# Kernel tuning notes

Measured on AMD Instinct MI355X. Metric: run time of the kernel, lower is better.

## Reference

```python
import math
import jax, jax.numpy as jnp
import numpy as np

NUM_HEAD = 16


def setup_inputs() -> dict:
    key = jax.random.key(0)
    k1, k2, k3, k4 = jax.random.split(key, 4)
    B, N, E = 64, 577, 1024
    x = jax.random.normal(k1, (B, N, E), dtype=jnp.float32)
    # nn.Linear weights are [out, in]; applied as x @ W.T. Scale like torch init.
    s = 1.0 / math.sqrt(E)
    Wq = jax.random.normal(k2, (E, E), dtype=jnp.float32) * s
    Wk = jax.random.normal(k3, (E, E), dtype=jnp.float32) * s
    Wv = jax.random.normal(k4, (E, E), dtype=jnp.float32) * s
    return {"x": x, "Wq": Wq, "Wk": Wk, "Wv": Wv}


def reference(x, Wq, Wk, Wv):
    B, N, E = x.shape
    H = NUM_HEAD
    D = E // H
    # QKV projections (bias=False), split heads -> [B, H, N, D]
    def proj(W):
        return (x @ W.T).reshape(B, N, H, D).transpose(0, 2, 1, 3)
    q, k, v = proj(Wq), proj(Wk), proj(Wv)
    # scaled dot-product attention (eval mode: dropout_p = 0)
    scale = 1.0 / math.sqrt(D)
    scores = jnp.einsum("bhnd,bhmd->bhnm", q, k) * scale
    probs = jax.nn.softmax(scores, axis=-1)
    out = jnp.einsum("bhnm,bhmd->bhnd", probs, v)
    # merge heads -> [B, N, E]
    return out.transpose(0, 2, 1, 3).reshape(B, N, E)
```

## Files before the change

### kernel.cpp

```cpp
#include <hip/hip_runtime.h>
#include <hip/hip_bf16.h>


typedef __attribute__((ext_vector_type(8))) short s16x8;
typedef __attribute__((ext_vector_type(4))) float f32x4;
typedef __attribute__((ext_vector_type(16))) float f32x16;
typedef __attribute__((ext_vector_type(4))) unsigned int u32x4;
typedef __attribute__((ext_vector_type(2))) unsigned int u32x2;

#define MFMA16(a, b, c) __builtin_amdgcn_mfma_f32_16x16x32_bf16((a), (b), (c), 0, 0, 0)
#define MFMA32(a, b, c) __builtin_amdgcn_mfma_f32_32x32x16_bf16((a), (b), (c), 0, 0, 0)

__device__ __forceinline__ short f2bf(float f) {
    unsigned u = __builtin_bit_cast(unsigned, f);
    u += 0x7FFFu + ((u >> 16) & 1u);
    return (short)(u >> 16);
}

__device__ __forceinline__ unsigned cvtpk(float lo, float hi) {
    unsigned r;
    asm("v_cvt_pk_bf16_f32 %0, %1, %2" : "=v"(r) : "v"(lo), "v"(hi));
    return r;
}

__device__ __forceinline__ void gload_lds16(const void* g, void* l) {
    __builtin_amdgcn_global_load_lds(
        (const __attribute__((address_space(1))) unsigned int*)g,
        (__attribute__((address_space(3))) unsigned int*)l,
        16, 0, 0);
}

__global__ __launch_bounds__(256) void convert_bf16(
    const float* __restrict__ x,
    const float* __restrict__ Wq,
    const float* __restrict__ Wk,
    const float* __restrict__ Wv,
    short* __restrict__ xb,
    short* __restrict__ Wb)
{
    constexpr size_t NX = 37814272u / 8u;
    constexpr size_t NW = 1048576u / 8u;
    constexpr size_t NTOT = NX + 3u * NW;
    size_t stride = (size_t)gridDim.x * blockDim.x;
    for (size_t c = (size_t)blockIdx.x * blockDim.x + threadIdx.x; c < NTOT; c += stride) {
        const float* src;
        short* dst;
        size_t off;
        if (c < NX) { src = x; off = c * 8; dst = xb + off; }
        else {
            size_t cw = c - NX;
            int wsel = (int)(cw / NW);
            src = (wsel == 0) ? Wq : (wsel == 1) ? Wk : Wv;
            off = (cw - (size_t)wsel * NW) * 8;
            dst = Wb + cw * 8;
        }
        float4 a0 = *reinterpret_cast<const float4*>(src + off);
        float4 a1 = *reinterpret_cast<const float4*>(src + off + 4);
        s16x8 v;
        v[0]=f2bf(a0.x); v[1]=f2bf(a0.y); v[2]=f2bf(a0.z); v[3]=f2bf(a0.w);
        v[4]=f2bf(a1.x); v[5]=f2bf(a1.y); v[6]=f2bf(a1.z); v[7]=f2bf(a1.w);
        *reinterpret_cast<s16x8*>(dst) = v;
    }
}

__global__ __launch_bounds__(512, 2) void qkv_gemm4(
    const short* __restrict__ xb,
    const short* __restrict__ Wb,
    short* __restrict__ Qb,
    short* __restrict__ Kb,
    short* __restrict__ Vb)
{
    constexpr int M = 36928;
    constexpr int NT = 12;
    constexpr int NWG = 145 * NT;
    __shared__ char LDS[131072];

    const int t    = threadIdx.x;
    const int lane = t & 63;
    const int w    = t >> 6;
    const int wr   = w >> 2, wc = w & 3;
    const int ml   = lane & 15, zz = lane >> 4;

    int orig = blockIdx.x;
    int xcd  = orig & 7;
    constexpr int QO = NWG / 8, RO = NWG % 8;
    int id = (xcd < RO ? xcd * (QO + 1) : RO * (QO + 1) + (xcd - RO) * QO) + (orig >> 3);
    const int tileM = (id / NT) * 256;
    const int tileN = (id % NT) * 256;

    const char* Ab = (const char*)xb;
    const char* Bb = (const char*)Wb;

    int s_row[2], s_lcol[2], s_arow[2];
    #pragma unroll
    for (int p = 0; p < 2; ++p) {
        int u = p * 512 + t;
        int row = u >> 2;
        int physu = u & 3;
        s_row[p]  = row;
        s_lcol[p] = ((physu ^ ((row >> 1) & 3)) << 4);
        int ar = tileM + row; if (ar > M - 1) ar = M - 1;
        s_arow[p] = ar;
    }

    #define REGOFF(buf_, op_, ks_) ((buf_) * 65536 + (op_) * 32768 + (ks_) * 16384)

    #define STAGE(tt_, op_, ks_, buf_)                                          \
    {   _Pragma("unroll")                                                       \
        for (int p = 0; p < 2; ++p) {                                           \
            int u = p * 512 + t;                                                \
            size_t gb;                                                          \
            if ((op_) == 0) gb = (size_t)s_arow[p] * 2048 + (tt_) * 128 + (ks_) * 64 + s_lcol[p]; \
            else            gb = (size_t)(tileN + s_row[p]) * 2048 + (tt_) * 128 + (ks_) * 64 + s_lcol[p]; \
            gload_lds16((((op_) == 0) ? Ab : Bb) + gb,                          \
                        LDS + REGOFF(buf_, op_, ks_) + u * 16);                 \
        } }

    auto rdA = [&](int buf, int ks, int mf) {
        int row = wr * 128 + mf * 16 + ml;
        int off = REGOFF(buf, 0, ks) + row * 64 + ((zz ^ ((row >> 1) & 3)) << 4);
        return *reinterpret_cast<const s16x8*>(LDS + off);
    };
    auto rdB = [&](int buf, int ks, int nf) {
        int row = wc * 64 + nf * 16 + ml;
        int off = REGOFF(buf, 1, ks) + row * 64 + ((zz ^ ((row >> 1) & 3)) << 4);
        return *reinterpret_cast<const s16x8*>(LDS + off);
    };

    #define RD_A(dst_, buf_, mb_)                                  \
    {   _Pragma("unroll")                                          \
        for (int mf2 = 0; mf2 < 4; ++mf2) {                        \
            dst_[mf2*2+0] = rdA(buf_, 0, (mb_)+mf2);               \
            dst_[mf2*2+1] = rdA(buf_, 1, (mb_)+mf2);               \
        } }
    #define RD_B(dst_, buf_, nb_)                                  \
    {   _Pragma("unroll")                                          \
        for (int nf2 = 0; nf2 < 2; ++nf2) {                        \
            dst_[nf2*2+0] = rdB(buf_, 0, (nb_)+nf2);               \
            dst_[nf2*2+1] = rdB(buf_, 1, (nb_)+nf2);               \
        } }

    #define QMFMA(AF_, BF_, MH_, NH_)                              \
    {   __builtin_amdgcn_s_setprio(1);                             \
        _Pragma("unroll")                                          \
        for (int mf2 = 0; mf2 < 4; ++mf2)                          \
            _Pragma("unroll")                                      \
            for (int nf2 = 0; nf2 < 2; ++nf2)                      \
                acc[(MH_)*4+mf2][(NH_)*2+nf2] =                    \
                    MFMA16(AF_[mf2*2+0], BF_[nf2*2+0], acc[(MH_)*4+mf2][(NH_)*2+nf2]); \
        _Pragma("unroll")                                          \
        for (int mf2 = 0; mf2 < 4; ++mf2)                          \
            _Pragma("unroll")                                      \
            for (int nf2 = 0; nf2 < 2; ++nf2)                      \
                acc[(MH_)*4+mf2][(NH_)*2+nf2] =                    \
                    MFMA16(AF_[mf2*2+1], BF_[nf2*2+1], acc[(MH_)*4+mf2][(NH_)*2+nf2]); \
        __builtin_amdgcn_s_setprio(0); }

    f32x4 acc[8][4] = {};
    s16x8 aC[8], aN[8], bC[4], bN[4];

    STAGE(0, 0, 0, 0); STAGE(0, 1, 0, 0); STAGE(0, 0, 1, 0); STAGE(0, 1, 1, 0);
    asm volatile("s_waitcnt vmcnt(0)" ::: "memory");
    __builtin_amdgcn_s_barrier();
    __builtin_amdgcn_sched_barrier(0);
    RD_A(aC, 0, 0);
    RD_B(bC, 0, 0);

    for (int tt = 0; tt < 16; ++tt) {
        const int buf = tt & 1, nbuf = buf ^ 1;
        const bool pre = (tt < 15);

        asm volatile("s_waitcnt lgkmcnt(0)" ::: "memory");
        __builtin_amdgcn_sched_barrier(0);
        if (pre) { STAGE(tt + 1, 0, 0, nbuf); STAGE(tt + 1, 1, 0, nbuf); }
        RD_B(bN, buf, 2);
        RD_A(aN, buf, 4);
        QMFMA(aC, bC, 0, 0);

        asm volatile("s_waitcnt lgkmcnt(8)" ::: "memory");
        __builtin_amdgcn_sched_barrier(0);
        if (pre) { STAGE(tt + 1, 0, 1, nbuf); STAGE(tt + 1, 1, 1, nbuf); }
        QMFMA(aC, bN, 0, 1);

        asm volatile("s_waitcnt lgkmcnt(0)" ::: "memory");
        __builtin_amdgcn_sched_barrier(0);
        QMFMA(aN, bC, 1, 0);

        asm volatile("s_waitcnt vmcnt(0)" ::: "memory");
        __builtin_amdgcn_s_barrier();
        __builtin_amdgcn_sched_barrier(0);
        if (pre) { RD_A(aC, nbuf, 0); RD_B(bC, nbuf, 0); }
        QMFMA(aN, bN, 1, 1);
    }

    const int z2 = tileN >> 10;
    short* Ob = (z2 == 0) ? Qb : (z2 == 1) ? Kb : Vb;
    const int cbase = (tileN & 1023) + wc * 64;

    #pragma unroll
    for (int mf = 0; mf < 8; ++mf) {
        #pragma unroll
        for (int j = 0; j < 4; ++j) {
            int row = tileM + wr * 128 + mf * 16 + zz * 4 + j;
            if (row < M) {
                int b = row / 577;
                int n = row - b * 577;
                #pragma unroll
                for (int nf = 0; nf < 4; ++nf) {
                    int cz = cbase + nf * 16 + ml;
                    int h = cz >> 6, dd = cz & 63;
                    Ob[(((size_t)(b * 16 + h)) * 577 + n) * 64 + dd] = f2bf(acc[mf][nf][j]);
                }
            }
        }
    }
    #undef STAGE
    #undef REGOFF
    #undef RD_A
    #undef RD_B
    #undef QMFMA
}

__global__ __launch_bounds__(256) void vtrans(
    const short* __restrict__ Vb,
    short* __restrict__ Vt)
{
    __shared__ short lds[64 * 64];
    const int t  = threadIdx.x;
    const int n0 = blockIdx.x * 64;
    const int bh = blockIdx.y;
    const size_t slab  = (size_t)bh * (577 * 64);
    const size_t vslab = (size_t)bh * (64 * 584);

    int r  = t >> 2;
    int d0 = (t & 3) * 16;
    int row = n0 + r; if (row > 576) row = 576;
    const short* src = Vb + slab + (size_t)row * 64 + d0;
    s16x8 v0 = *reinterpret_cast<const s16x8*>(src);
    s16x8 v1 = *reinterpret_cast<const s16x8*>(src + 8);
    #pragma unroll
    for (int j = 0; j < 8; ++j) {
        lds[(d0 + j) * 64 + r]     = v0[j];
        lds[(d0 + 8 + j) * 64 + r] = v1[j];
    }
    __syncthreads();
    #pragma unroll
    for (int p = 0; p < 2; ++p) {
        int u  = p * 256 + t;
        int dd = u >> 3, ns = u & 7;
        int n  = n0 + ns * 8;
        if (n < 584) {
            s16x8 vv = *reinterpret_cast<const s16x8*>(&lds[dd * 64 + ns * 8]);
            *reinterpret_cast<s16x8*>(Vt + vslab + (size_t)dd * 584 + n) = vv;
        }
    }
}

__global__ __launch_bounds__(256, 4) void attn_fwd5(
    const short* __restrict__ Qb,
    const short* __restrict__ Kb,
    const short* __restrict__ Vt,
    float* __restrict__ out)
{
    constexpr int   N    = 577;
    constexpr float CEXP = 0.18033688011112042f;

    __shared__ short K_lds[2][4096];
    __shared__ short V_lds[2][4096];

    const int t     = threadIdx.x;
    const int lane  = t & 63;
    const int w     = t >> 6;
    const int col_q = lane & 31;
    const int hi    = lane >> 5;
    const int hi8   = hi * 8;
    const int c7    = col_q & 7;

    int bd  = blockIdx.x;
    int xx  = bd & 7;
    int r_  = bd >> 3;
    int qt  = r_ % 5;
    int bh  = (r_ / 5) * 8 + xx;
    const int bB = bh >> 4, hH = bh & 15;
    const size_t slab  = (size_t)bh * (N * 64);
    const size_t vslab = (size_t)bh * (64 * 584);

    const int q0 = qt * 128 + w * 32;

    s16x8 qb[4];
    {
        int qr = q0 + col_q; if (qr > N - 1) qr = N - 1;
        const short* qrow = Qb + slab + (size_t)qr * 64 + hi8;
        #pragma unroll
        for (int ks = 0; ks < 4; ++ks)
            qb[ks] = *reinterpret_cast<const s16x8*>(qrow + ks * 16);
    }

    const int sr = t >> 3;
    const int sp = t & 7;

    float m_run = -1e30f, l_run = 0.f;
    f32x16 o0 = {}, o1 = {};

    #pragma unroll
    for (int p = 0; p < 2; ++p) {
        int rr = p * 32 + sr;
        int sl = sp ^ (rr & 7);
        gload_lds16(Kb + slab + (size_t)rr * 64 + sl * 8, &K_lds[0][(rr * 8 + sp) * 8]);
        gload_lds16(Vt + vslab + (size_t)rr * 584 + sl * 8, &V_lds[0][(rr * 8 + sp) * 8]);
    }
    int cur = 0;

    for (int tile = 0; tile < 10; ++tile) {
        const int kv0 = tile * 64;
        __builtin_amdgcn_sched_barrier(0);
        __builtin_amdgcn_s_barrier();
        if (tile < 9) {
            #pragma unroll
            for (int p = 0; p < 2; ++p) {
                int rr = p * 32 + sr;
                int sl = sp ^ (rr & 7);
                gload_lds16(Kb + slab + (size_t)(kv0 + 64 + rr) * 64 + sl * 8,
                            &K_lds[cur ^ 1][(rr * 8 + sp) * 8]);
                gload_lds16(Vt + vslab + (size_t)rr * 584 + (kv0 + 64) + sl * 8,
                            &V_lds[cur ^ 1][(rr * 8 + sp) * 8]);
            }
            asm volatile("s_waitcnt vmcnt(4)" ::: "memory");
        } else {
            asm volatile("s_waitcnt vmcnt(0)" ::: "memory");
        }
        __builtin_amdgcn_sched_barrier(0);

        const short* KL = &K_lds[cur][0];
        const short* VL = &V_lds[cur][0];

        f32x16 s0 = {}, s1 = {};
        __builtin_amdgcn_s_setprio(1);
        #pragma unroll
        for (int ks = 0; ks < 4; ++ks) {
            s16x8 kf0 = *reinterpret_cast<const s16x8*>(
                KL + ((col_q * 8 + ((2*ks + hi) ^ c7)) * 8));
            s0 = MFMA32(kf0, qb[ks], s0);
        }
        #pragma unroll
        for (int ks = 0; ks < 4; ++ks) {
            s16x8 kf1 = *reinterpret_cast<const s16x8*>(
                KL + (((32 + col_q) * 8 + ((2*ks + hi) ^ c7)) * 8));
            s1 = MFMA32(kf1, qb[ks], s1);
        }
        __builtin_amdgcn_s_setprio(0);

        if (kv0 + 64 > N) {
            #pragma unroll
            for (int r = 0; r < 16; ++r) {
                int crow = (r & 3) + 8 * (r >> 2) + 4 * hi;
                if (kv0 + crow > N - 1) s0[r] = -1e30f;
                s1[r] = -1e30f;
            }
        }

        float pm = s0[0];
        #pragma unroll
        for (int r = 1; r < 15; r += 2) pm = fmaxf(fmaxf(pm, s0[r]), s0[r+1]);
        pm = fmaxf(pm, s0[15]);
        #pragma unroll
        for (int r = 0; r < 16; r += 2) pm = fmaxf(fmaxf(pm, s1[r]), s1[r+1]);
        float pmax2 = fmaxf(pm, __shfl_xor(pm, 32));

        bool need = (pmax2 - m_run) * CEXP > 8.f;
        if (__ballot(need)) {
            float mn   = fmaxf(m_run, pmax2);
            float corr = exp2f(CEXP * (m_run - mn));
            m_run = mn;
            l_run *= corr;
            #pragma unroll
            for (int r = 0; r < 16; ++r) { o0[r] *= corr; o1[r] *= corr; }
        }
        float cmn = CEXP * m_run;

        float psum = 0.f;
        #pragma unroll
        for (int r = 0; r < 16; ++r) { s0[r] = exp2f(__builtin_fmaf(s0[r], CEXP, -cmn)); psum += s0[r]; }
        #pragma unroll
        for (int r = 0; r < 16; ++r) { s1[r] = exp2f(__builtin_fmaf(s1[r], CEXP, -cmn)); psum += s1[r]; }
        l_run += psum + __shfl_xor(psum, 32);

        #define REPACK(S_, b_, dst_)                                              \
        {   u32x2 r1_ = __builtin_amdgcn_permlane32_swap(                         \
                cvtpk(S_[(b_)+0], S_[(b_)+1]), cvtpk(S_[(b_)+4], S_[(b_)+5]), false, false); \
            u32x2 r2_ = __builtin_amdgcn_permlane32_swap(                         \
                cvtpk(S_[(b_)+2], S_[(b_)+3]), cvtpk(S_[(b_)+6], S_[(b_)+7]), false, false); \
            dst_[0] = r1_[0]; dst_[2] = r1_[1]; dst_[1] = r2_[0]; dst_[3] = r2_[1]; }

        #define PVSTEP(ks_, S_, b_)                                               \
        {   u32x4 pwk_;                                                           \
            REPACK(S_, b_, pwk_);                                                 \
            s16x8 paf_ = __builtin_bit_cast(s16x8, pwk_);                         \
            s16x8 vf0_ = *reinterpret_cast<const s16x8*>(                         \
                VL + ((col_q * 8 + ((2*(ks_) + hi) ^ c7)) * 8));                  \
            o0 = MFMA32(vf0_, paf_, o0);                                          \
            s16x8 vf1_ = *reinterpret_cast<const s16x8*>(                         \
                VL + (((32 + col_q) * 8 + ((2*(ks_) + hi) ^ c7)) * 8));           \
            o1 = MFMA32(vf1_, paf_, o1);                                          \
        }

        __builtin_amdgcn_s_setprio(1);
        PVSTEP(0, s0, 0)
        PVSTEP(1, s0, 8)
        PVSTEP(2, s1, 0)
        PVSTEP(3, s1, 8)
        __builtin_amdgcn_s_setprio(0);
        #undef PVSTEP
        #undef REPACK
        cur ^= 1;
    }

    int q = q0 + col_q;
    if (q < N) {
        float inv = 1.0f / l_run;
        float* obase = out + ((size_t)bB * 577 + q) * 1024 + (size_t)hH * 64;
        #pragma unroll
        for (int gq = 0; gq < 4; ++gq) {
            float4 v0 = { o0[4*gq+0]*inv, o0[4*gq+1]*inv, o0[4*gq+2]*inv, o0[4*gq+3]*inv };
            *reinterpret_cast<float4*>(obase + 8*gq + 4*hi) = v0;
            float4 v1 = { o1[4*gq+0]*inv, o1[4*gq+1]*inv, o1[4*gq+2]*inv, o1[4*gq+3]*inv };
            *reinterpret_cast<float4*>(obase + 32 + 8*gq + 4*hi) = v1;
        }
    }
}

extern "C" void kernel_launch(void* const* d_in, const int* in_sizes, int n_in,
                              void* d_out, int out_size, void* d_ws, size_t ws_size,
                              hipStream_t stream) {
    const float* x  = (const float*)d_in[0];
    const float* Wq = (const float*)d_in[1];
    const float* Wk = (const float*)d_in[2];
    const float* Wv = (const float*)d_in[3];
    float* out = (float*)d_out;

    const size_t SZ   = (size_t)64 * 16 * 577 * 64 * 2;
    const size_t VTSZ = (size_t)1024 * 64 * 584 * 2;
    short* Qb = (short*)d_ws;
    short* Kb = (short*)((char*)d_ws + SZ);
    short* Vt = (short*)((char*)d_ws + 2 * SZ);
    short* Wb = (short*)((char*)d_ws + 2 * SZ + VTSZ);

    short* xb = (short*)d_out;
    short* Vb = (short*)((char*)d_out + SZ);

    convert_bf16<<<2048, 256, 0, stream>>>(x, Wq, Wk, Wv, xb, Wb);
    qkv_gemm4<<<dim3(145 * 12), 512, 0, stream>>>(xb, Wb, Qb, Kb, Vb);
    vtrans<<<dim3(10, 1024), 256, 0, stream>>>(Vb, Vt);
    attn_fwd5<<<5120, 256, 0, stream>>>(Qb, Kb, Vt, out);
}
```

Measured before the change: 499.3 us.

## Fold softmax scale into Wq and restructure GEMM main loop with finer barriers

```diff
diff --git a/kernel.cpp b/kernel.cpp
--- a/kernel.cpp
+++ b/kernel.cpp
@@ -46,24 +46,26 @@
         const float* src;
         short* dst;
         size_t off;
+        float scale = 1.0f;
         if (c < NX) { src = x; off = c * 8; dst = xb + off; }
         else {
             size_t cw = c - NX;
             int wsel = (int)(cw / NW);
             src = (wsel == 0) ? Wq : (wsel == 1) ? Wk : Wv;
+            if (wsel == 0) scale = 0.18033688011112042f;
             off = (cw - (size_t)wsel * NW) * 8;
             dst = Wb + cw * 8;
         }
         float4 a0 = *reinterpret_cast<const float4*>(src + off);
         float4 a1 = *reinterpret_cast<const float4*>(src + off + 4);
         s16x8 v;
-        v[0]=f2bf(a0.x); v[1]=f2bf(a0.y); v[2]=f2bf(a0.z); v[3]=f2bf(a0.w);
-        v[4]=f2bf(a1.x); v[5]=f2bf(a1.y); v[6]=f2bf(a1.z); v[7]=f2bf(a1.w);
+        v[0]=f2bf(a0.x*scale); v[1]=f2bf(a0.y*scale); v[2]=f2bf(a0.z*scale); v[3]=f2bf(a0.w*scale);
+        v[4]=f2bf(a1.x*scale); v[5]=f2bf(a1.y*scale); v[6]=f2bf(a1.z*scale); v[7]=f2bf(a1.w*scale);
         *reinterpret_cast<s16x8*>(dst) = v;
     }
 }
 
-__global__ __launch_bounds__(512, 2) void qkv_gemm4(
+__global__ __launch_bounds__(512, 2) void qkv_gemm5(
     const short* __restrict__ xb,
     const short* __restrict__ Wb,
     short* __restrict__ Qb,
@@ -163,34 +165,43 @@
     asm volatile("s_waitcnt vmcnt(0)" ::: "memory");
     __builtin_amdgcn_s_barrier();
     __builtin_amdgcn_sched_barrier(0);
-    RD_A(aC, 0, 0);
-    RD_B(bC, 0, 0);
 
     for (int tt = 0; tt < 16; ++tt) {
         const int buf = tt & 1, nbuf = buf ^ 1;
         const bool pre = (tt < 15);
 
+        RD_A(aC, buf, 0);
+        RD_B(bC, buf, 0);
+        if (pre) STAGE(tt + 1, 0, 0, nbuf);
+        __builtin_amdgcn_s_barrier();
         asm volatile("s_waitcnt lgkmcnt(0)" ::: "memory");
         __builtin_amdgcn_sched_barrier(0);
-        if (pre) { STAGE(tt + 1, 0, 0, nbuf); STAGE(tt + 1, 1, 0, nbuf); }
+        QMFMA(aC, bC, 0, 0);
+        __builtin_amdgcn_s_barrier();
+
         RD_B(bN, buf, 2);
+        if (pre) STAGE(tt + 1, 1, 0, nbuf);
+        __builtin_amdgcn_s_barrier();
+        asm volatile("s_waitcnt lgkmcnt(0)" ::: "memory");
+        __builtin_amdgcn_sched_barrier(0);
+        QMFMA(aC, bN, 0, 1);
+        __builtin_amdgcn_s_barrier();
+
         RD_A(aN, buf, 4);
-        QMFMA(aC, bC, 0, 0);
-
-        asm volatile("s_waitcnt lgkmcnt(8)" ::: "memory");
-        __builtin_amdgcn_sched_barrier(0);
-        if (pre) { STAGE(tt + 1, 0, 1, nbuf); STAGE(tt + 1, 1, 1, nbuf); }
-        QMFMA(aC, bN, 0, 1);
-
+        if (pre) STAGE(tt + 1, 0, 1, nbuf);
+        __builtin_amdgcn_s_barrier();
         asm volatile("s_waitcnt lgkmcnt(0)" ::: "memory");
         __builtin_amdgcn_sched_barrier(0);
         QMFMA(aN, bC, 1, 0);
-
+        __builtin_amdgcn_s_barrier();
+
+        if (pre) STAGE(tt + 1, 1, 1, nbuf);
+        __builtin_amdgcn_s_barrier();
+        __builtin_amdgcn_sched_barrier(0);
+        QMFMA(aN, bN, 1, 1);
         asm volatile("s_waitcnt vmcnt(0)" ::: "memory");
         __builtin_amdgcn_s_barrier();
         __builtin_amdgcn_sched_barrier(0);
-        if (pre) { RD_A(aC, nbuf, 0); RD_B(bC, nbuf, 0); }
-        QMFMA(aN, bN, 1, 1);
     }
 
     const int z2 = tileN >> 10;
@@ -256,14 +267,13 @@
     }
 }
 
-__global__ __launch_bounds__(256, 4) void attn_fwd5(
+__global__ __launch_bounds__(256, 4) void attn_fwd6(
     const short* __restrict__ Qb,
     const short* __restrict__ Kb,
     const short* __restrict__ Vt,
     float* __restrict__ out)
 {
-    constexpr int   N    = 577;
-    constexpr float CEXP = 0.18033688011112042f;
+    constexpr int N = 577;
 
     __shared__ short K_lds[2][4096];
     __shared__ short V_lds[2][4096];
@@ -367,22 +377,22 @@
         for (int r = 0; r < 16; r += 2) pm = fmaxf(fmaxf(pm, s1[r]), s1[r+1]);
         float pmax2 = fmaxf(pm, __shfl_xor(pm, 32));
 
-        bool need = (pmax2 - m_run) * CEXP > 8.f;
+        bool need = (pmax2 - m_run) > 8.f;
         if (__ballot(need)) {
             float mn   = fmaxf(m_run, pmax2);
-            float corr = exp2f(CEXP * (m_run - mn));
+            float corr = exp2f(m_run - mn);
             m_run = mn;
             l_run *= corr;
             #pragma unroll
             for (int r = 0; r < 16; ++r) { o0[r] *= corr; o1[r] *= corr; }
         }
-        float cmn = CEXP * m_run;
+        float cmn = m_run;
 
         float psum = 0.f;
         #pragma unroll
-        for (int r = 0; r < 16; ++r) { s0[r] = exp2f(__builtin_fmaf(s0[r], CEXP, -cmn)); psum += s0[r]; }
-        #pragma unroll
-        for (int r = 0; r < 16; ++r) { s1[r] = exp2f(__builtin_fmaf(s1[r], CEXP, -cmn)); psum += s1[r]; }
+        for (int r = 0; r < 16; ++r) { s0[r] = exp2f(s0[r] - cmn); psum += s0[r]; }
+        #pragma unroll
+        for (int r = 0; r < 16; ++r) { s1[r] = exp2f(s1[r] - cmn); psum += s1[r]; }
         l_run += psum + __shfl_xor(psum, 32);
 
         #define REPACK(S_, b_, dst_)                                              \
@@ -449,7 +459,7 @@
     short* Vb = (short*)((char*)d_out + SZ);
 
     convert_bf16<<<2048, 256, 0, stream>>>(x, Wq, Wk, Wv, xb, Wb);
-    qkv_gemm4<<<dim3(145 * 12), 512, 0, stream>>>(xb, Wb, Qb, Kb, Vb);
+    qkv_gemm5<<<dim3(145 * 12), 512, 0, stream>>>(xb, Wb, Qb, Kb, Vb);
     vtrans<<<dim3(10, 1024), 256, 0, stream>>>(Vb, Vt);
-    attn_fwd5<<<5120, 256, 0, stream>>>(Qb, Kb, Vt, out);
-}
+    attn_fwd6<<<5120, 256, 0, stream>>>(Qb, Kb, Vt, out);
+}
```

Result: faster. 487.6 us (-2.3%).
